# Kernel tuning notes

Hardware: AMD Instinct MI355X
Metric: run time of the kernel (lower is better)

## Reference

```python
import jax, jax.numpy as jnp
import numpy as np

N, DEG, F_IN, HID, OUT = 20000, 16, 128, 128, 64
E = N * DEG


def setup_inputs() -> dict:
    key = jax.random.key(0)
    ks = jax.random.split(key, 12)
    s = 0.05  # small init scale to keep activations stable
    x = jax.random.normal(ks[0], (N, F_IN), jnp.float32)
    # PyG LSTM aggregation requires edges sorted by destination; fixed degree DEG
    src = jax.random.randint(ks[1], (E,), 0, N, dtype=jnp.int32)
    dst = jnp.repeat(jnp.arange(N, dtype=jnp.int32), DEG)
    edge_index = jnp.stack([src, dst])  # [2, E]
    return {
        "x": x,
        "edge_index": edge_index,
        "lstm_Wih": jax.random.normal(ks[2], (4, 4 * HID, F_IN), jnp.float32) * s,
        "lstm_Whh": jax.random.normal(ks[3], (4, 4 * HID, HID), jnp.float32) * s,
        "lstm_bih": jax.random.normal(ks[4], (4, 4 * HID), jnp.float32) * s,
        "lstm_bhh": jax.random.normal(ks[5], (4, 4 * HID), jnp.float32) * s,
        "linl_W123": jax.random.normal(ks[6], (3, HID, HID), jnp.float32) * s,
        "linl_b123": jax.random.normal(ks[7], (3, HID), jnp.float32) * s,
        "linr_W123": jax.random.normal(ks[8], (3, HID, HID), jnp.float32) * s,
        "linl_W4": jax.random.normal(ks[9], (OUT, HID), jnp.float32) * s,
        "linl_b4": jax.random.normal(ks[10], (OUT,), jnp.float32) * s,
        "linr_W4": jax.random.normal(ks[11], (OUT, HID), jnp.float32) * s,
    }


def _lstm_last(msgs, Wih, Whh, bih, bhh):
    """Run an LSTM over the padded neighbor sequence, return h at last step.
    msgs: [n, deg, f]. Matches PyG LSTMAggregation (lstm(x)[0][:, -1])."""
    n = msgs.shape[0]
    H = Whh.shape[1]
    b = bih + bhh  # torch LSTM adds both biases

    def step(carry, xt):  # xt: [n, f]
        h, c = carry
        g = xt @ Wih.T + h @ Whh.T + b  # [n, 4H], gate order i,f,g,o
        i, f, gg, o = jnp.split(g, 4, axis=-1)
        c = jax.nn.sigmoid(f) * c + jax.nn.sigmoid(i) * jnp.tanh(gg)
        h = jax.nn.sigmoid(o) * jnp.tanh(c)
        return (h, c), None

    h0 = jnp.zeros((n, H), msgs.dtype)
    (h, _), _ = jax.lax.scan(step, (h0, h0), jnp.swapaxes(msgs, 0, 1))
    return h


def _sage_conv(x, src, Wih, Whh, bih, bhh, Wl, bl, Wr):
    """SAGEConv(aggr='lstm'): lin_l(lstm_agg(x_j)) + lin_r(x).
    Fixed degree + dst-sorted edges => to_dense_batch is a reshape."""
    n, f = x.shape
    msgs = x[src].reshape(n, DEG, f)  # gather neighbor (source) features
    agg = _lstm_last(msgs, Wih, Whh, bih, bhh)
    return agg @ Wl.T + bl + x @ Wr.T  # lin_r has no bias in PyG


def reference(x, edge_index, lstm_Wih, lstm_Whh, lstm_bih, lstm_bhh,
              linl_W123, linl_b123, linr_W123, linl_W4, linl_b4, linr_W4):
    src = edge_index[0]
    # eval mode: dropout is identity
    x1 = jax.nn.relu(_sage_conv(x, src, lstm_Wih[0], lstm_Whh[0], lstm_bih[0],
                                lstm_bhh[0], linl_W123[0], linl_b123[0], linr_W123[0]))
    x2 = jax.nn.relu(_sage_conv(x1, src, lstm_Wih[1], lstm_Whh[1], lstm_bih[1],
                                lstm_bhh[1], linl_W123[1], linl_b123[1], linr_W123[1]) + x1)
    x3 = jax.nn.relu(_sage_conv(x2, src, lstm_Wih[2], lstm_Whh[2], lstm_bih[2],
                                lstm_bhh[2], linl_W123[2], linl_b123[2], linr_W123[2]) + x2)
    x4 = _sage_conv(x3, src, lstm_Wih[3], lstm_Whh[3], lstm_bih[3], lstm_bhh[3],
                    linl_W4, linl_b4, linr_W4)
    return x4
```

## Files before the change

### kernel.cpp

```cpp
#include <hip/hip_runtime.h>


#define N_NODES 20000
#define DEG 16

typedef __bf16 bf16x8 __attribute__((ext_vector_type(8)));
typedef float f32x4 __attribute__((ext_vector_type(4)));

__device__ inline unsigned short f2bf(float f) {
  unsigned u = __builtin_bit_cast(unsigned, f);
  u += 0x7fffu + ((u >> 16) & 1u);
  return (unsigned short)(u >> 16);
}
__device__ inline float fexp2(float x) {
#if __has_builtin(__builtin_amdgcn_exp2f)
  return __builtin_amdgcn_exp2f(x);
#else
  return exp2f(x);
#endif
}
__device__ inline float frcp(float x) {
#if __has_builtin(__builtin_amdgcn_rcpf)
  return __builtin_amdgcn_rcpf(x);
#else
  return 1.f / x;
#endif
}
__device__ inline float sigm(float x) { return frcp(1.f + fexp2(-1.44269504f * x)); }
__device__ inline float tanh_(float x) { return frcp(1.f + fexp2(-2.88539008f * x)) * 2.f - 1.f; }

__global__ __launch_bounds__(256) void prep_weights(
    const float* __restrict__ Wih, const float* __restrict__ Whh,
    const float* __restrict__ bih, const float* __restrict__ bhh,
    unsigned short* __restrict__ WihB, unsigned short* __restrict__ WhhB,
    float* __restrict__ bsum) {
  int tid = blockIdx.x * 256 + threadIdx.x;
  float4 a = *(const float4*)(Wih + tid * 4);
  ushort4 o;
  o.x = f2bf(a.x); o.y = f2bf(a.y); o.z = f2bf(a.z); o.w = f2bf(a.w);
  *(ushort4*)(WihB + tid * 4) = o;
  float4 b = *(const float4*)(Whh + tid * 4);
  ushort4 p;
  p.x = f2bf(b.x); p.y = f2bf(b.y); p.z = f2bf(b.z); p.w = f2bf(b.w);
  *(ushort4*)(WhhB + tid * 4) = p;
  if (tid < 2048) bsum[tid] = bih[tid] + bhh[tid];
}

__global__ __launch_bounds__(256) void cast_bf(
    const float* __restrict__ x, unsigned short* __restrict__ xb) {
  int tid = blockIdx.x * 256 + threadIdx.x;
  float4 v = *(const float4*)(x + tid * 4);
  ushort4 o;
  o.x = f2bf(v.x); o.y = f2bf(v.y); o.z = f2bf(v.z); o.w = f2bf(v.w);
  *(ushort4*)(xb + tid * 4) = o;
}

__global__ __launch_bounds__(512) void lstm_fused(
    const unsigned short* __restrict__ xbf,
    const int* __restrict__ src,
    const unsigned short* __restrict__ WihB,
    const unsigned short* __restrict__ WhhB,
    const float* __restrict__ bsum,
    float* __restrict__ agg) {
  __shared__ __align__(16) unsigned char xs[256 * 256];
  __shared__ __align__(16) unsigned char hbuf[2][16 * 256];
  __shared__ __align__(16) int idx_s[256];
  const int tid = threadIdx.x;
  const int lane = tid & 63, w = tid >> 6;
  const int l15 = lane & 15, l4 = lane >> 4;
  const int node0 = blockIdx.x * 16;
  const int colb = w * 16 + l15;

  if (tid < 256) idx_s[(tid & 15) * 16 + (tid >> 4)] = src[node0 * DEG + tid];
  __syncthreads();

#pragma unroll
  for (int it = 0; it < 8; ++it) {
    int e = w * 32 + it * 4 + l4;
    int idx = idx_s[e];
    uint4 v = *(const uint4*)(xbf + idx * 128 + l15 * 8);
    int byte = (e * 256 + l15 * 16) ^ ((e & 7) << 4);
    *(uint4*)(xs + byte) = v;
  }

  bf16x8 bwx[4][4], bwh[4][4];
  float bs[4];
#pragma unroll
  for (int g = 0; g < 4; ++g) {
#pragma unroll
    for (int kt = 0; kt < 4; ++kt) {
      bwx[g][kt] = *(const bf16x8*)(WihB + (g * 128 + colb) * 128 + kt * 32 + l4 * 8);
      bwh[g][kt] = *(const bf16x8*)(WhhB + (g * 128 + colb) * 128 + kt * 32 + l4 * 8);
    }
    bs[g] = bsum[g * 128 + colb];
  }
  __syncthreads();

  float c[4] = {0.f, 0.f, 0.f, 0.f};

#pragma unroll
  for (int t = 0; t < 16; ++t) {
    f32x4 acc[4];
#pragma unroll
    for (int g = 0; g < 4; ++g) acc[g] = (f32x4){bs[g], bs[g], bs[g], bs[g]};

    {
      bf16x8 afx[4];
#pragma unroll
      for (int kt = 0; kt < 4; ++kt) {
        int e = t * 16 + l15;
        int byte = (e * 256 + kt * 64 + l4 * 16) ^ ((e & 7) << 4);
        afx[kt] = *(const bf16x8*)(xs + byte);
      }
#pragma unroll
      for (int g = 0; g < 4; ++g)
#pragma unroll
        for (int kt = 0; kt < 4; ++kt)
          acc[g] = __builtin_amdgcn_mfma_f32_16x16x32_bf16(afx[kt], bwx[g][kt],
                                                           acc[g], 0, 0, 0);
    }

    if (t > 0) {
      const unsigned char* hb = hbuf[(t - 1) & 1];
      bf16x8 afh[4];
#pragma unroll
      for (int kt = 0; kt < 4; ++kt) {
        int byte = (l15 * 256 + kt * 64 + l4 * 16) ^ ((l15 & 7) << 4);
        afh[kt] = *(const bf16x8*)(hb + byte);
      }
#pragma unroll
      for (int g = 0; g < 4; ++g)
#pragma unroll
        for (int kt = 0; kt < 4; ++kt)
          acc[g] = __builtin_amdgcn_mfma_f32_16x16x32_bf16(afh[kt], bwh[g][kt],
                                                           acc[g], 0, 0, 0);
    }

    float hn[4];
#pragma unroll
    for (int r = 0; r < 4; ++r) {
      float ig = sigm(acc[0][r]), fg = sigm(acc[1][r]);
      float gg = tanh_(acc[2][r]), og = sigm(acc[3][r]);
      float cn = fg * c[r] + ig * gg;
      c[r] = cn;
      hn[r] = og * tanh_(cn);
    }

    if (t < 15) {
      unsigned char* hw = hbuf[t & 1];
#pragma unroll
      for (int r = 0; r < 4; ++r) {
        int m = l4 * 4 + r;
        int byte = (m * 256 + colb * 2) ^ ((m & 7) << 4);
        *(__bf16*)(hw + byte) = (__bf16)hn[r];
      }
      __syncthreads();
    } else {
#pragma unroll
      for (int r = 0; r < 4; ++r)
        agg[(node0 + l4 * 4 + r) * 128 + colb] = hn[r];
    }
  }
}

__global__ __launch_bounds__(256) void gemm_out(
    const float* __restrict__ A1,
    const float* __restrict__ A2,
    const float* __restrict__ Wl, const float* __restrict__ bl,
    const float* __restrict__ Wr,
    const float* __restrict__ resid,
    float* __restrict__ out,
    unsigned short* __restrict__ outbf,
    int NOUT, int do_relu, int Nrows) {
  __shared__ __align__(16) unsigned char As[64 * 512];
  const int tid = threadIdx.x;
  const int lane = tid & 63, w = tid >> 6;
  const int l15 = lane & 15, l4 = lane >> 4;
  const int row0 = blockIdx.x * 64;

#pragma unroll
  for (int i = 0; i < 16; ++i) {
    int flat = i * 1024 + tid * 4;
    int r = flat >> 8, c = flat & 255;
    int grow = row0 + r;
    float4 v;
    if (grow < Nrows)
      v = (c < 128) ? *(const float4*)(A1 + grow * 128 + c)
                    : *(const float4*)(A2 + grow * 128 + (c - 128));
    else
      v = make_float4(0.f, 0.f, 0.f, 0.f);
    ushort4 b;
    b.x = f2bf(v.x); b.y = f2bf(v.y); b.z = f2bf(v.z); b.w = f2bf(v.w);
    int byte = (r * 512 + c * 2) ^ ((r & 7) << 4);
    *(ushort4*)(As + byte) = b;
  }
  __syncthreads();

  const int colg = blockIdx.y * 64 + w * 16 + l15;
  bf16x8 bw[8];
#pragma unroll
  for (int kt = 0; kt < 8; ++kt) {
    const float* bp = (kt < 4) ? (Wl + colg * 128 + kt * 32 + l4 * 8)
                               : (Wr + colg * 128 + (kt - 4) * 32 + l4 * 8);
    float4 a = *(const float4*)bp;
    float4 b = *(const float4*)(bp + 4);
    bf16x8 v;
    v[0] = (__bf16)a.x; v[1] = (__bf16)a.y; v[2] = (__bf16)a.z; v[3] = (__bf16)a.w;
    v[4] = (__bf16)b.x; v[5] = (__bf16)b.y; v[6] = (__bf16)b.z; v[7] = (__bf16)b.w;
    bw[kt] = v;
  }

  f32x4 acc[4];
#pragma unroll
  for (int rt = 0; rt < 4; ++rt) acc[rt] = (f32x4){0.f, 0.f, 0.f, 0.f};

#pragma unroll
  for (int kt = 0; kt < 8; ++kt) {
#pragma unroll
    for (int rt = 0; rt < 4; ++rt) {
      int m = rt * 16 + l15;
      int byte = (m * 512 + kt * 64 + l4 * 16) ^ ((m & 7) << 4);
      bf16x8 af = *(const bf16x8*)(As + byte);
      acc[rt] = __builtin_amdgcn_mfma_f32_16x16x32_bf16(af, bw[kt], acc[rt], 0, 0, 0);
    }
  }

  const float bias = bl[colg];
#pragma unroll
  for (int rt = 0; rt < 4; ++rt)
#pragma unroll
    for (int r = 0; r < 4; ++r) {
      int grow = row0 + rt * 16 + l4 * 4 + r;
      if (grow < Nrows) {
        float v = acc[rt][r] + bias;
        if (resid) v += resid[grow * 128 + colg];
        if (do_relu) v = fmaxf(v, 0.f);
        out[grow * NOUT + colg] = v;
        if (outbf) outbf[grow * 128 + colg] = f2bf(v);
      }
    }
}

extern "C" void kernel_launch(void* const* d_in, const int* in_sizes, int n_in,
                              void* d_out, int out_size, void* d_ws, size_t ws_size,
                              hipStream_t stream) {
  const float* X = (const float*)d_in[0];
  const int* src = (const int*)d_in[1];
  const float* Wih = (const float*)d_in[2];
  const float* Whh = (const float*)d_in[3];
  const float* bih = (const float*)d_in[4];
  const float* bhh = (const float*)d_in[5];
  const float* Wl123 = (const float*)d_in[6];
  const float* bl123 = (const float*)d_in[7];
  const float* Wr123 = (const float*)d_in[8];
  const float* Wl4 = (const float*)d_in[9];
  const float* bl4 = (const float*)d_in[10];
  const float* Wr4 = (const float*)d_in[11];
  float* out = (float*)d_out;

  char* ws = (char*)d_ws;
  unsigned short* xbf = (unsigned short*)ws;
  float* agg = (float*)(ws + 5120000);
  float* xb0 = (float*)(ws + 15360000);
  float* xb1 = (float*)(ws + 25600000);
  unsigned short* WihB = (unsigned short*)(ws + 35840000);
  unsigned short* WhhB = (unsigned short*)(ws + 36364288);
  float* bsumW = (float*)(ws + 36888576);

  prep_weights<<<dim3(256), 256, 0, stream>>>(Wih, Whh, bih, bhh, WihB, WhhB, bsumW);
  cast_bf<<<dim3(2500), 256, 0, stream>>>(X, xbf);

  const float* xcur = X;
  for (int L = 0; L < 4; ++L) {
    lstm_fused<<<dim3(1250), 512, 0, stream>>>(xbf, src, WihB + L * 65536,
                                               WhhB + L * 65536, bsumW + L * 512, agg);
    if (L < 3) {
      float* nxt = (L & 1) ? xb1 : xb0;
      gemm_out<<<dim3(313, 2), 256, 0, stream>>>(agg, xcur, Wl123 + L * 16384,
                                                 bl123 + L * 128, Wr123 + L * 16384,
                                                 (L >= 1) ? xcur : nullptr, nxt, xbf,
                                                 128, 1, N_NODES);
      xcur = nxt;
    } else {
      gemm_out<<<dim3(313, 1), 256, 0, stream>>>(agg, xcur, Wl4, bl4, Wr4, nullptr, out,
                                                 nullptr, 64, 0, N_NODES);
    }
  }
}
```

Measured before the change: 563.5 us.

## Load gathered neighbor features directly into registers with one-step prefetch

Removes the 64KB shared-memory staging buffer for all gathered neighbor rows. Each wave now loads the bf16 features for the next timestep from global memory straight into MFMA operand registers, overlapping that load with the current step's compute. This frees LDS, which could raise occupancy, and removes an upfront barrier and LDS round trip. The cost is that every wave re-gathers the same rows redundantly (8 waves each load the whole 16x128 tile per step), increasing L2 traffic and register pressure.

Result: slower. 688.7 us (+22.2%).

```diff
diff --git a/kernel.cpp b/kernel.cpp
--- a/kernel.cpp
+++ b/kernel.cpp
@@ -62,7 +62,6 @@
     const unsigned short* __restrict__ WhhB,
     const float* __restrict__ bsum,
     float* __restrict__ agg) {
-  __shared__ __align__(16) unsigned char xs[256 * 256];
   __shared__ __align__(16) unsigned char hbuf[2][16 * 256];
   __shared__ __align__(16) int idx_s[256];
   const int tid = threadIdx.x;
@@ -72,16 +71,6 @@
   const int colb = w * 16 + l15;
 
   if (tid < 256) idx_s[(tid & 15) * 16 + (tid >> 4)] = src[node0 * DEG + tid];
-  __syncthreads();
-
-#pragma unroll
-  for (int it = 0; it < 8; ++it) {
-    int e = w * 32 + it * 4 + l4;
-    int idx = idx_s[e];
-    uint4 v = *(const uint4*)(xbf + idx * 128 + l15 * 8);
-    int byte = (e * 256 + l15 * 16) ^ ((e & 7) << 4);
-    *(uint4*)(xs + byte) = v;
-  }
 
   bf16x8 bwx[4][4], bwh[4][4];
   float bs[4];
@@ -98,27 +87,33 @@
 
   float c[4] = {0.f, 0.f, 0.f, 0.f};
 
+#define LOADX(T, DST)                                                  \
+  {                                                                    \
+    int idx = idx_s[(T) * 16 + l15];                                   \
+    const unsigned short* rp = xbf + idx * 128 + l4 * 8;               \
+    DST[0] = *(const bf16x8*)(rp);                                     \
+    DST[1] = *(const bf16x8*)(rp + 32);                                \
+    DST[2] = *(const bf16x8*)(rp + 64);                                \
+    DST[3] = *(const bf16x8*)(rp + 96);                                \
+  }
+
+  bf16x8 xc[4], xn[4];
+  LOADX(0, xc)
+
 #pragma unroll
   for (int t = 0; t < 16; ++t) {
+    if (t < 15) LOADX(t + 1, xn)
+
     f32x4 acc[4];
 #pragma unroll
     for (int g = 0; g < 4; ++g) acc[g] = (f32x4){bs[g], bs[g], bs[g], bs[g]};
 
-    {
-      bf16x8 afx[4];
-#pragma unroll
-      for (int kt = 0; kt < 4; ++kt) {
-        int e = t * 16 + l15;
-        int byte = (e * 256 + kt * 64 + l4 * 16) ^ ((e & 7) << 4);
-        afx[kt] = *(const bf16x8*)(xs + byte);
-      }
-#pragma unroll
-      for (int g = 0; g < 4; ++g)
-#pragma unroll
-        for (int kt = 0; kt < 4; ++kt)
-          acc[g] = __builtin_amdgcn_mfma_f32_16x16x32_bf16(afx[kt], bwx[g][kt],
-                                                           acc[g], 0, 0, 0);
-    }
+#pragma unroll
+    for (int g = 0; g < 4; ++g)
+#pragma unroll
+      for (int kt = 0; kt < 4; ++kt)
+        acc[g] = __builtin_amdgcn_mfma_f32_16x16x32_bf16(xc[kt], bwx[g][kt],
+                                                         acc[g], 0, 0, 0);
 
     if (t > 0) {
       const unsigned char* hb = hbuf[(t - 1) & 1];
@@ -155,12 +150,15 @@
         *(__bf16*)(hw + byte) = (__bf16)hn[r];
       }
       __syncthreads();
+#pragma unroll
+      for (int kt = 0; kt < 4; ++kt) xc[kt] = xn[kt];
     } else {
 #pragma unroll
       for (int r = 0; r < 4; ++r)
         agg[(node0 + l4 * 4 + r) * 128 + colb] = hn[r];
     }
   }
+#undef LOADX
 }
 
 __global__ __launch_bounds__(256) void gemm_out(
```

## Process 32 nodes per LSTM block and stream neighbor gathers per timestep

Applied to the files above, without the earlier changes.

Each LSTM block now handles 32 nodes (two 16-row MFMA tiles) rather than 16, so the register-resident weight fragments are reused across twice as many rows and the grid halves. The whole upfront neighbor gather into a 64KB shared buffer is replaced by a double-buffered per-timestep gather: the next step's neighbor rows are loaded into registers while the current step's MFMAs run, then stored to shared memory before the barrier. Shared memory per block drops, and with launch_bounds(512,2) two blocks may fit per CU. The cost is more register pressure from doubled accumulators and cell state, plus reduced grid parallelism with only 625 blocks.

Result: faster. 549.5 us (-2.5%).

```diff
diff --git a/kernel.cpp b/kernel.cpp
--- a/kernel.cpp
+++ b/kernel.cpp
@@ -55,33 +55,23 @@
   *(ushort4*)(xb + tid * 4) = o;
 }
 
-__global__ __launch_bounds__(512) void lstm_fused(
+__global__ __launch_bounds__(512, 2) void lstm_fused(
     const unsigned short* __restrict__ xbf,
     const int* __restrict__ src,
     const unsigned short* __restrict__ WihB,
     const unsigned short* __restrict__ WhhB,
     const float* __restrict__ bsum,
     float* __restrict__ agg) {
-  __shared__ __align__(16) unsigned char xs[256 * 256];
-  __shared__ __align__(16) unsigned char hbuf[2][16 * 256];
-  __shared__ __align__(16) int idx_s[256];
+  __shared__ __align__(16) unsigned char xsb[2][32 * 256];
+  __shared__ __align__(16) unsigned char hbuf[2][32 * 256];
+  __shared__ __align__(16) int idx_s[512];
   const int tid = threadIdx.x;
   const int lane = tid & 63, w = tid >> 6;
   const int l15 = lane & 15, l4 = lane >> 4;
-  const int node0 = blockIdx.x * 16;
+  const int node0 = blockIdx.x * 32;
   const int colb = w * 16 + l15;
 
-  if (tid < 256) idx_s[(tid & 15) * 16 + (tid >> 4)] = src[node0 * DEG + tid];
-  __syncthreads();
-
-#pragma unroll
-  for (int it = 0; it < 8; ++it) {
-    int e = w * 32 + it * 4 + l4;
-    int idx = idx_s[e];
-    uint4 v = *(const uint4*)(xbf + idx * 128 + l15 * 8);
-    int byte = (e * 256 + l15 * 16) ^ ((e & 7) << 4);
-    *(uint4*)(xs + byte) = v;
-  }
+  idx_s[(tid & 15) * 32 + (tid >> 4)] = src[node0 * DEG + tid];
 
   bf16x8 bwx[4][4], bwh[4][4];
   float bs[4];
@@ -96,69 +86,99 @@
   }
   __syncthreads();
 
-  float c[4] = {0.f, 0.f, 0.f, 0.f};
-
-#pragma unroll
+  const int erow = w * 4 + l4;
+  const int schunk = l15 ^ (erow & 7);
+
+  {
+    int idx = idx_s[erow];
+    uint4 v = *(const uint4*)(xbf + idx * 128 + schunk * 8);
+    *(uint4*)(&xsb[0][erow * 256 + l15 * 16]) = v;
+  }
+  __syncthreads();
+
+  float c[2][4] = {{0.f, 0.f, 0.f, 0.f}, {0.f, 0.f, 0.f, 0.f}};
+
   for (int t = 0; t < 16; ++t) {
-    f32x4 acc[4];
-#pragma unroll
-    for (int g = 0; g < 4; ++g) acc[g] = (f32x4){bs[g], bs[g], bs[g], bs[g]};
-
-    {
+    uint4 xstg;
+    if (t < 15) {
+      int idx = idx_s[(t + 1) * 32 + erow];
+      xstg = *(const uint4*)(xbf + idx * 128 + schunk * 8);
+    }
+
+    const unsigned char* xrb = xsb[t & 1];
+    f32x4 acc[2][4];
+#pragma unroll
+    for (int rt = 0; rt < 2; ++rt)
+#pragma unroll
+      for (int g = 0; g < 4; ++g) acc[rt][g] = (f32x4){bs[g], bs[g], bs[g], bs[g]};
+
+#pragma unroll
+    for (int rt = 0; rt < 2; ++rt) {
       bf16x8 afx[4];
 #pragma unroll
       for (int kt = 0; kt < 4; ++kt) {
-        int e = t * 16 + l15;
-        int byte = (e * 256 + kt * 64 + l4 * 16) ^ ((e & 7) << 4);
-        afx[kt] = *(const bf16x8*)(xs + byte);
+        int m = rt * 16 + l15;
+        int byte = (m * 256 + kt * 64 + l4 * 16) ^ ((m & 7) << 4);
+        afx[kt] = *(const bf16x8*)(xrb + byte);
       }
 #pragma unroll
       for (int g = 0; g < 4; ++g)
 #pragma unroll
         for (int kt = 0; kt < 4; ++kt)
-          acc[g] = __builtin_amdgcn_mfma_f32_16x16x32_bf16(afx[kt], bwx[g][kt],
-                                                           acc[g], 0, 0, 0);
+          acc[rt][g] = __builtin_amdgcn_mfma_f32_16x16x32_bf16(afx[kt], bwx[g][kt],
+                                                               acc[rt][g], 0, 0, 0);
     }
 
     if (t > 0) {
       const unsigned char* hb = hbuf[(t - 1) & 1];
-      bf16x8 afh[4];
-#pragma unroll
-      for (int kt = 0; kt < 4; ++kt) {
-        int byte = (l15 * 256 + kt * 64 + l4 * 16) ^ ((l15 & 7) << 4);
-        afh[kt] = *(const bf16x8*)(hb + byte);
+#pragma unroll
+      for (int rt = 0; rt < 2; ++rt) {
+        bf16x8 afh[4];
+#pragma unroll
+        for (int kt = 0; kt < 4; ++kt) {
+          int m = rt * 16 + l15;
+          int byte = (m * 256 + kt * 64 + l4 * 16) ^ ((m & 7) << 4);
+          afh[kt] = *(const bf16x8*)(hb + byte);
+        }
+#pragma unroll
+        for (int g = 0; g < 4; ++g)
+#pragma unroll
+          for (int kt = 0; kt < 4; ++kt)
+            acc[rt][g] = __builtin_amdgcn_mfma_f32_16x16x32_bf16(afh[kt], bwh[g][kt],
+                                                                 acc[rt][g], 0, 0, 0);
       }
-#pragma unroll
-      for (int g = 0; g < 4; ++g)
-#pragma unroll
-        for (int kt = 0; kt < 4; ++kt)
-          acc[g] = __builtin_amdgcn_mfma_f32_16x16x32_bf16(afh[kt], bwh[g][kt],
-                                                           acc[g], 0, 0, 0);
-    }
-
-    float hn[4];
-#pragma unroll
-    for (int r = 0; r < 4; ++r) {
-      float ig = sigm(acc[0][r]), fg = sigm(acc[1][r]);
-      float gg = tanh_(acc[2][r]), og = sigm(acc[3][r]);
-      float cn = fg * c[r] + ig * gg;
-      c[r] = cn;
-      hn[r] = og * tanh_(cn);
-    }
+    }
+
+    float hn[2][4];
+#pragma unroll
+    for (int rt = 0; rt < 2; ++rt)
+#pragma unroll
+      for (int r = 0; r < 4; ++r) {
+        float ig = sigm(acc[rt][0][r]), fg = sigm(acc[rt][1][r]);
+        float gg = tanh_(acc[rt][2][r]), og = sigm(acc[rt][3][r]);
+        float cn = fg * c[rt][r] + ig * gg;
+        c[rt][r] = cn;
+        hn[rt][r] = og * tanh_(cn);
+      }
 
     if (t < 15) {
       unsigned char* hw = hbuf[t & 1];
 #pragma unroll
-      for (int r = 0; r < 4; ++r) {
-        int m = l4 * 4 + r;
-        int byte = (m * 256 + colb * 2) ^ ((m & 7) << 4);
-        *(__bf16*)(hw + byte) = (__bf16)hn[r];
-      }
+      for (int rt = 0; rt < 2; ++rt)
+#pragma unroll
+        for (int r = 0; r < 4; ++r) {
+          int m = rt * 16 + l4 * 4 + r;
+          int byte = (m * 256 + colb * 2) ^ ((m & 7) << 4);
+          *(__bf16*)(hw + byte) = (__bf16)hn[rt][r];
+        }
+      *(uint4*)(&xsb[(t + 1) & 1][erow * 256 + l15 * 16]) = xstg;
       __syncthreads();
     } else {
 #pragma unroll
-      for (int r = 0; r < 4; ++r)
-        agg[(node0 + l4 * 4 + r) * 128 + colb] = hn[r];
+      for (int rt = 0; rt < 2; ++rt)
+#pragma unroll
+        for (int r = 0; r < 4; ++r)
+          agg[(node0 + rt * 16 + l4 * 4 + r) * 128 + colb] = hn[rt][r];
     }
   }
 }
@@ -272,8 +292,8 @@
 
   const float* xcur = X;
   for (int L = 0; L < 4; ++L) {
-    lstm_fused<<<dim3(1250), 512, 0, stream>>>(xbf, src, WihB + L * 65536,
-                                               WhhB + L * 65536, bsumW + L * 512, agg);
+    lstm_fused<<<dim3(625), 512, 0, stream>>>(xbf, src, WihB + L * 65536,
+                                              WhhB + L * 65536, bsumW + L * 512, agg);
     if (L < 3) {
       float* nxt = (L & 1) ? xb1 : xb0;
       gemm_out<<<dim3(313, 2), 256, 0, stream>>>(agg, xcur, Wl123 + L * 16384,
```
